# Performance work log

Hardware: AMD Instinct MI355X
Metric: run time of the kernel (lower is better)

Reference implementation:

```python
import jax, jax.numpy as jnp
import numpy as np

KQ_D = 64  # head dim from init_kwargs

def setup_inputs() -> dict:
    key = jax.random.key(0)
    k1, k2, k3, k4 = jax.random.split(key, 4)
    B, H, S, D = 2, 12, 2048, KQ_D
    q = jax.random.normal(k1, (B, H, S, D), dtype=jnp.float32)
    k = jax.random.normal(k2, (B, H, S, D), dtype=jnp.float32)
    v = jax.random.normal(k3, (B, H, S, D), dtype=jnp.float32)
    mask = jax.random.randint(k4, (B, 1, S, S), 0, 2, dtype=jnp.int32)
    return {"q": q, "k": k, "v": v, "mask": mask}

def reference(q, k, v, mask):
    # attn = (q @ k^T) / sqrt(kq_d)
    scale = 1.0 / (KQ_D ** 0.5)
    attn = jnp.einsum('bhqd,bhkd->bhqk', q, k) * scale
    # masked_fill(mask == 0, -1e9)
    attn = jnp.where(mask == 0, jnp.float32(-1e9), attn)
    # softmax over keys; dropout is identity in eval/reference mode
    attn = jax.nn.softmax(attn, axis=-1)
    out = jnp.einsum('bhqk,bhkd->bhqd', attn, v)
    return out
```

## Files before the change

### kernel.cpp

```cpp
#include <hip/hip_runtime.h>
#include <hip/hip_bf16.h>

#define S_LEN 2048
#define D_DIM 64
#define NH    12
#define NB    2
#define BH_N  (NB*NH)
#define TILES 32
#define TILE_BYTES 16384
#define KV_WS_BYTES ((size_t)BH_N * TILES * TILE_BYTES)
#define MASK_WORDS  ((size_t)NB * S_LEN * TILES)
#define WS_NEEDED   (KV_WS_BYTES + MASK_WORDS * 8)

typedef __attribute__((ext_vector_type(8))) short short8;
typedef __attribute__((ext_vector_type(4))) float f32x4;

static __device__ inline unsigned bfbits(float f) {
    __hip_bfloat16 h = __float2bfloat16(f);
    return (unsigned)*reinterpret_cast<const unsigned short*>(&h);
}

static __device__ inline void gload_lds16(const void* g, unsigned ldsoff) {
    __builtin_amdgcn_global_load_lds(
        (__attribute__((address_space(1))) void*)(unsigned long long)(uintptr_t)g,
        (__attribute__((address_space(3))) void*)(unsigned long long)ldsoff,
        16, 0, 0);
}

__global__ __launch_bounds__(256) void prep(const float* __restrict__ k,
                                            const float* __restrict__ v,
                                            const int* __restrict__ mask,
                                            char* __restrict__ wsKV,
                                            unsigned long long* __restrict__ wm) {
    __shared__ __align__(16) float sv[64 * 68];
    const int tid = threadIdx.x;
    const int bid = blockIdx.x;
    if (bid < 768) {
        const int t = bid & 31, bh = bid >> 5;
        const int kv0 = t * 64;
        const float* kb = k + (size_t)bh * (S_LEN * D_DIM);
        const float* vb = v + (size_t)bh * (S_LEN * D_DIM);
        char* img = wsKV + ((size_t)bh * TILES + t) * TILE_BYTES;

#pragma unroll
        for (int g = 0; g < 4; ++g) {
            int i = g * 256 + tid;
            int row = i >> 4, cb = (i & 15) << 3;
            int cp = cb ^ ((row & 7) << 4);
            float4 f = *(const float4*)(kb + (size_t)(kv0 + row) * D_DIM + (cp >> 1));
            uint2 u;
            u.x = bfbits(f.x) | (bfbits(f.y) << 16);
            u.y = bfbits(f.z) | (bfbits(f.w) << 16);
            *(uint2*)(img + (size_t)i * 8) = u;
            float4 fv = *(const float4*)(vb + (size_t)(kv0 + row) * D_DIM + ((i & 15) << 2));
            *(float4*)&sv[row * 68 + ((i & 15) << 2)] = fv;
        }
        __syncthreads();
#pragma unroll
        for (int g = 0; g < 4; ++g) {
            int i = g * 256 + tid;
            int drow = i >> 4, cb = (i & 15) << 3;
            int cp = cb ^ ((drow & 7) << 4);
            int key0 = cp >> 1;
            uint2 u;
            u.x = bfbits(sv[(key0 + 0) * 68 + drow]) | (bfbits(sv[(key0 + 1) * 68 + drow]) << 16);
            u.y = bfbits(sv[(key0 + 2) * 68 + drow]) | (bfbits(sv[(key0 + 3) * 68 + drow]) << 16);
            *(uint2*)(img + 8192 + (size_t)i * 8) = u;
        }
    } else {
        const int lane = tid & 63;
        const int wgid = (bid - 768) * 4 + (tid >> 6);
#pragma unroll 1
        for (int g = 0; g < 16; ++g) {
            const int t0 = wgid * 64 + g * 4;
            const size_t base = (size_t)t0 * 64 + lane;
            int m0 = mask[base];
            int m1 = mask[base + 64];
            int m2 = mask[base + 128];
            int m3 = mask[base + 192];
            unsigned long long b0 = __ballot(m0 != 0);
            unsigned long long b1 = __ballot(m1 != 0);
            unsigned long long b2 = __ballot(m2 != 0);
            unsigned long long b3 = __ballot(m3 != 0);
            if (lane == 0) {
                wm[t0 + 0] = b0; wm[t0 + 1] = b1;
                wm[t0 + 2] = b2; wm[t0 + 3] = b3;
            }
        }
    }
}

__global__ __launch_bounds__(256, 3) void attn_main(
    const float* __restrict__ q, const char* __restrict__ wsKV,
    const unsigned long long* __restrict__ wm, float* __restrict__ out)
{
    __shared__ __align__(16) char smem[2 * TILE_BYTES + 8192];

    const int tid  = threadIdx.x;
    const int wave = tid >> 6;
    const int lane = tid & 63;
    const int l16  = lane & 15;
    const int lhi  = lane >> 4;

    const int f  = blockIdx.x;
    const int n  = (f & 7) * 96 + (f >> 3);
    const int bx = n & 31;
    const int bh = n >> 5;
    const int b  = bh / NH;
    const int qw = bx * 64 + wave * 16;
    const int qq = qw + l16;

    const float* qb = q + (size_t)bh * (S_LEN * D_DIM);
    float*       ob = out + (size_t)bh * (S_LEN * D_DIM);
    const char*  tileBase = wsKV + (size_t)bh * TILES * TILE_BYTES;
    const size_t widx = ((size_t)b * S_LEN + qq) * TILES;

    const float PRE = 0.125f * 1.44269504088896f;

    short8 bq[2];
#pragma unroll
    for (int ks = 0; ks < 2; ++ks) {
        const float* src = qb + (size_t)qq * D_DIM + ks * 32 + lhi * 8;
        float4 f0 = *(const float4*)(src);
        float4 f1 = *(const float4*)(src + 4);
        short8 a;
        a[0] = (short)bfbits(f0.x * PRE); a[1] = (short)bfbits(f0.y * PRE);
        a[2] = (short)bfbits(f0.z * PRE); a[3] = (short)bfbits(f0.w * PRE);
        a[4] = (short)bfbits(f1.x * PRE); a[5] = (short)bfbits(f1.y * PRE);
        a[6] = (short)bfbits(f1.z * PRE); a[7] = (short)bfbits(f1.w * PRE);
        bq[ks] = a;
    }

    f32x4 o[4];
#pragma unroll
    for (int dt = 0; dt < 4; ++dt) o[dt] = (f32x4){0.f, 0.f, 0.f, 0.f};
    float lsum = 0.f;

    const unsigned smem_base = (unsigned)(uintptr_t)(&smem[0]);
    char* pw = smem + 2 * TILE_BYTES + wave * 2048;

    unsigned long long mw = wm[widx];
#pragma unroll
    for (int j = 0; j < 4; ++j) {
        unsigned off = (unsigned)(wave * 4096 + j * 1024 + lane * 16);
        gload_lds16(tileBase + off, smem_base + off);
    }
    __syncthreads();

    int buf = 0;
    for (int t = 0; t < 32; ++t) {
        if (t < 31) {
            const char* timg = tileBase + (size_t)(t + 1) * TILE_BYTES;
            unsigned dstb = smem_base + (unsigned)((buf ^ 1) * TILE_BYTES);
#pragma unroll
            for (int j = 0; j < 4; ++j) {
                unsigned off = (unsigned)(wave * 4096 + j * 1024 + lane * 16);
                gload_lds16(timg + off, dstb + off);
            }
        }
        unsigned long long mw_next = (t < 31) ? wm[widx + t + 1] : 0ull;

        const char* sK  = smem + buf * TILE_BYTES;
        const char* sVt = sK + 8192;

        f32x4 sc[4];
#pragma unroll
        for (int tt = 0; tt < 4; ++tt) sc[tt] = (f32x4){0.f, 0.f, 0.f, 0.f};
#pragma unroll
        for (int ks = 0; ks < 2; ++ks) {
#pragma unroll
            for (int tt = 0; tt < 4; ++tt) {
                int row = tt * 16 + l16;
                int byte = row * 128 + ((ks * 64 + lhi * 16) ^ ((row & 7) << 4));
                short8 ak = *(const short8*)(sK + byte);
                sc[tt] = __builtin_amdgcn_mfma_f32_16x16x32_bf16(ak, bq[ks], sc[tt], 0, 0, 0);
            }
        }

        short8 bvv[2][4];
#pragma unroll
        for (int ks = 0; ks < 2; ++ks)
#pragma unroll
            for (int dt = 0; dt < 4; ++dt) {
                int drow = dt * 16 + l16;
                int vbyte = drow * 128 + ((ks * 64 + lhi * 16) ^ ((drow & 7) << 4));
                bvv[ks][dt] = *(const short8*)(sVt + vbyte);
            }

        float rs = 0.f;
#pragma unroll
        for (int tt = 0; tt < 4; ++tt) {
            unsigned nib = (unsigned)(mw >> (tt * 16 + lhi * 4)) & 0xFu;
#pragma unroll
            for (int r = 0; r < 4; ++r) {
                float s = ((nib >> r) & 1u) ? sc[tt][r] : -1e9f;
                float p = exp2f(s);
                sc[tt][r] = p;
                rs += p;
            }
        }
        lsum += rs;

#pragma unroll
        for (int tt = 0; tt < 4; ++tt) {
            uint2 u;
            u.x = bfbits(sc[tt][0]) | (bfbits(sc[tt][1]) << 16);
            u.y = bfbits(sc[tt][2]) | (bfbits(sc[tt][3]) << 16);
            int byte = l16 * 128 + (((tt * 16 + lhi * 4) * 2) ^ ((l16 & 7) << 4));
            *(uint2*)(pw + byte) = u;
        }

#pragma unroll
        for (int ks = 0; ks < 2; ++ks) {
            int pbyte = l16 * 128 + ((ks * 64 + lhi * 16) ^ ((l16 & 7) << 4));
            short8 pa = *(const short8*)(pw + pbyte);
#pragma unroll
            for (int dt = 0; dt < 4; ++dt)
                o[dt] = __builtin_amdgcn_mfma_f32_16x16x32_bf16(pa, bvv[ks][dt], o[dt], 0, 0, 0);
        }

        __syncthreads();
        buf ^= 1;
        mw = mw_next;
    }

    lsum += __shfl_xor(lsum, 16);
    lsum += __shfl_xor(lsum, 32);
    float invl = 1.0f / lsum;
    float ir[4];
#pragma unroll
    for (int r = 0; r < 4; ++r) ir[r] = __shfl(invl, lhi * 4 + r);
#pragma unroll
    for (int dt = 0; dt < 4; ++dt)
#pragma unroll
        for (int r = 0; r < 4; ++r) {
            int qrow = qw + lhi * 4 + r;
            int dcol = dt * 16 + l16;
            ob[(size_t)qrow * D_DIM + dcol] = o[dt][r] * ir[r];
        }
}

__global__ __launch_bounds__(256, 3) void attn_fallback(
    const float* __restrict__ q, const float* __restrict__ k,
    const float* __restrict__ v, const int* __restrict__ mask,
    float* __restrict__ out)
{
    __shared__ __align__(16) unsigned short sK[4096];
    __shared__ __align__(16) unsigned short sVt[4096];
    __shared__ __align__(16) unsigned short sP[4096];

    const int tid  = threadIdx.x;
    const int wave = tid >> 6;
    const int lane = tid & 63;
    const int l16  = lane & 15;
    const int lhi  = lane >> 4;

    const int bh = blockIdx.y;
    const int b  = bh / NH;
    const int q0 = blockIdx.x * 64;
    const int qw = q0 + wave * 16;
    const int qq = qw + l16;

    const float* qbase = q + (size_t)bh * S_LEN * D_DIM;
    const float* kbase = k + (size_t)bh * S_LEN * D_DIM;
    const float* vbase = v + (size_t)bh * S_LEN * D_DIM;
    const int*   mp = mask + (size_t)b * S_LEN * S_LEN + (size_t)qq * S_LEN;

    const float PRE = 0.125f * 1.44269504088896f;

    short8 bq[2];
#pragma unroll
    for (int ks = 0; ks < 2; ++ks) {
        const float* src = qbase + (size_t)qq * D_DIM + ks * 32 + lhi * 8;
        float4 f0 = *(const float4*)(src);
        float4 f1 = *(const float4*)(src + 4);
        short8 a;
        a[0] = (short)bfbits(f0.x * PRE); a[1] = (short)bfbits(f0.y * PRE);
        a[2] = (short)bfbits(f0.z * PRE); a[3] = (short)bfbits(f0.w * PRE);
        a[4] = (short)bfbits(f1.x * PRE); a[5] = (short)bfbits(f1.y * PRE);
        a[6] = (short)bfbits(f1.z * PRE); a[7] = (short)bfbits(f1.w * PRE);
        bq[ks] = a;
    }

    f32x4 o[4];
#pragma unroll
    for (int dt = 0; dt < 4; ++dt) o[dt] = (f32x4){0.f, 0.f, 0.f, 0.f};
    float mrun = -1e30f, lrun = 0.f;
    unsigned short* pw = sP + wave * 1024;

    int srow[4], sd[4];
#pragma unroll
    for (int s = 0; s < 4; ++s) { int i = tid + 256 * s; srow[s] = i >> 4; sd[s] = (i & 15) * 4; }

    float4 kreg[4], vreg[4];
#pragma unroll
    for (int s = 0; s < 4; ++s) {
        kreg[s] = *(const float4*)(kbase + (size_t)srow[s] * D_DIM + sd[s]);
        vreg[s] = *(const float4*)(vbase + (size_t)srow[s] * D_DIM + sd[s]);
    }

    for (int kv0 = 0; kv0 < S_LEN; kv0 += 64) {
        __syncthreads();
#pragma unroll
        for (int s = 0; s < 4; ++s) {
            unsigned p0 = bfbits(kreg[s].x) | (bfbits(kreg[s].y) << 16);
            unsigned p1 = bfbits(kreg[s].z) | (bfbits(kreg[s].w) << 16);
            int byte = srow[s] * 128 + ((sd[s] * 2) ^ ((srow[s] & 7) << 4));
            *(uint2*)((char*)sK + byte) = make_uint2(p0, p1);
        }
#pragma unroll
        for (int s = 0; s < 4; ++s) {
            float ff[4] = {vreg[s].x, vreg[s].y, vreg[s].z, vreg[s].w};
#pragma unroll
            for (int jj = 0; jj < 4; ++jj) {
                int dd = sd[s] + jj;
                int byte = dd * 128 + ((srow[s] * 2) ^ ((dd & 7) << 4));
                *(unsigned short*)((char*)sVt + byte) = (unsigned short)bfbits(ff[jj]);
            }
        }
        __syncthreads();

        if (kv0 + 64 < S_LEN) {
#pragma unroll
            for (int s = 0; s < 4; ++s) {
                kreg[s] = *(const float4*)(kbase + (size_t)(kv0 + 64 + srow[s]) * D_DIM + sd[s]);
                vreg[s] = *(const float4*)(vbase + (size_t)(kv0 + 64 + srow[s]) * D_DIM + sd[s]);
            }
        }

        int4 m0 = *(const int4*)(mp + kv0 + lhi * 4);
        int4 m1 = *(const int4*)(mp + kv0 + 16 + lhi * 4);
        int4 m2 = *(const int4*)(mp + kv0 + 32 + lhi * 4);
        int4 m3 = *(const int4*)(mp + kv0 + 48 + lhi * 4);

        f32x4 sc[4];
#pragma unroll
        for (int tt = 0; tt < 4; ++tt) sc[tt] = (f32x4){0.f, 0.f, 0.f, 0.f};
#pragma unroll
        for (int ks = 0; ks < 2; ++ks) {
#pragma unroll
            for (int tt = 0; tt < 4; ++tt) {
                int row = tt * 16 + l16;
                int byte = row * 128 + ((ks * 64 + lhi * 16) ^ ((row & 7) << 4));
                short8 ak = *(const short8*)((const char*)sK + byte);
                sc[tt] = __builtin_amdgcn_mfma_f32_16x16x32_bf16(ak, bq[ks], sc[tt], 0, 0, 0);
            }
        }

        const int4 mm[4] = {m0, m1, m2, m3};
        float pm = -1e30f;
#pragma unroll
        for (int tt = 0; tt < 4; ++tt)
#pragma unroll
            for (int r = 0; r < 4; ++r) {
                float s = ((const int*)&mm[tt])[r] ? sc[tt][r] : -1e9f;
                sc[tt][r] = s;
                pm = fmaxf(pm, s);
            }
        pm = fmaxf(pm, __shfl_xor(pm, 16));
        pm = fmaxf(pm, __shfl_xor(pm, 32));

        float mnew = fmaxf(mrun, pm);
        float fsc = exp2f(mrun - mnew);
        mrun = mnew;
        float rs = 0.f;
#pragma unroll
        for (int tt = 0; tt < 4; ++tt)
#pragma unroll
            for (int r = 0; r < 4; ++r) {
                float p = exp2f(sc[tt][r] - mnew);
                sc[tt][r] = p;
                rs += p;
            }
        rs += __shfl_xor(rs, 16);
        rs += __shfl_xor(rs, 32);
        lrun = lrun * fsc + rs;

        float fr[4];
#pragma unroll
        for (int r = 0; r < 4; ++r) fr[r] = __shfl(fsc, lhi * 4 + r);
#pragma unroll
        for (int dt = 0; dt < 4; ++dt)
#pragma unroll
            for (int r = 0; r < 4; ++r) o[dt][r] *= fr[r];

#pragma unroll
        for (int tt = 0; tt < 4; ++tt) {
            unsigned p0 = bfbits(sc[tt][0]) | (bfbits(sc[tt][1]) << 16);
            unsigned p1 = bfbits(sc[tt][2]) | (bfbits(sc[tt][3]) << 16);
            int byte = l16 * 128 + (((tt * 16 + lhi * 4) * 2) ^ ((l16 & 7) << 4));
            *(uint2*)((char*)pw + byte) = make_uint2(p0, p1);
        }

#pragma unroll
        for (int ks = 0; ks < 2; ++ks) {
            int pbyte = l16 * 128 + ((ks * 64 + lhi * 16) ^ ((l16 & 7) << 4));
            short8 pa = *(const short8*)((const char*)pw + pbyte);
#pragma unroll
            for (int dt = 0; dt < 4; ++dt) {
                int drow = dt * 16 + l16;
                int vbyte = drow * 128 + ((ks * 64 + lhi * 16) ^ ((drow & 7) << 4));
                short8 bv = *(const short8*)((const char*)sVt + vbyte);
                o[dt] = __builtin_amdgcn_mfma_f32_16x16x32_bf16(pa, bv, o[dt], 0, 0, 0);
            }
        }
    }

    float invl = 1.0f / lrun;
    float ir[4];
#pragma unroll
    for (int r = 0; r < 4; ++r) ir[r] = __shfl(invl, lhi * 4 + r);
#pragma unroll
    for (int dt = 0; dt < 4; ++dt)
#pragma unroll
        for (int r = 0; r < 4; ++r) {
            int qrow = qw + lhi * 4 + r;
            int dcol = dt * 16 + l16;
            out[(size_t)bh * S_LEN * D_DIM + (size_t)qrow * D_DIM + dcol] = o[dt][r] * ir[r];
        }
}

extern "C" void kernel_launch(void* const* d_in, const int* in_sizes, int n_in,
                              void* d_out, int out_size, void* d_ws, size_t ws_size,
                              hipStream_t stream) {
    const float* q   = (const float*)d_in[0];
    const float* k   = (const float*)d_in[1];
    const float* v   = (const float*)d_in[2];
    const int* mask  = (const int*)d_in[3];
    float* out = (float*)d_out;

    if (ws_size >= WS_NEEDED) {
        char* ws = (char*)d_ws;
        char* wsKV = ws;
        unsigned long long* wm = (unsigned long long*)(ws + KV_WS_BYTES);
        prep<<<dim3(1280), dim3(256), 0, stream>>>(k, v, mask, wsKV, wm);
        attn_main<<<dim3(768), dim3(256), 0, stream>>>(q, wsKV, wm, out);
    } else {
        attn_fallback<<<dim3(S_LEN / 64, BH_N), dim3(256), 0, stream>>>(q, k, v, mask, out);
    }
}
```

Before: 73.55 us.

## Switch attention main loop to 32x32x16 MFMA with split-K waves

Reworks the main attention kernel to use 32x32x16 bf16 MFMA instructions instead of 16x16x32. Waves are now split two ways over query rows and two ways over keys within each tile, and the two key-half partial outputs and row sums are merged through shared memory at the end. Exponentials for masked entries are skipped and P is written directly per group. The aim is fewer, larger MFMAs and fewer LDS reads per tile, at the cost of an extra LDS reduction and a sync in the epilogue.

```diff
diff --git a/kernel.cpp b/kernel.cpp
--- a/kernel.cpp
+++ b/kernel.cpp
@@ -14,6 +14,7 @@
 
 typedef __attribute__((ext_vector_type(8))) short short8;
 typedef __attribute__((ext_vector_type(4))) float f32x4;
+typedef __attribute__((ext_vector_type(16))) float f32x16;
 
 static __device__ inline unsigned bfbits(float f) {
     __hip_bfloat16 h = __float2bfloat16(f);
@@ -99,16 +100,18 @@
     const int tid  = threadIdx.x;
     const int wave = tid >> 6;
     const int lane = tid & 63;
-    const int l16  = lane & 15;
-    const int lhi  = lane >> 4;
+    const int l32  = lane & 31;
+    const int lh   = lane >> 5;
+    const int qh   = wave & 1;
+    const int kh   = wave >> 1;
 
     const int f  = blockIdx.x;
     const int n  = (f & 7) * 96 + (f >> 3);
     const int bx = n & 31;
     const int bh = n >> 5;
     const int b  = bh / NH;
-    const int qw = bx * 64 + wave * 16;
-    const int qq = qw + l16;
+    const int qw = bx * 64 + qh * 32;
+    const int qq = qw + l32;
 
     const float* qb = q + (size_t)bh * (S_LEN * D_DIM);
     float*       ob = out + (size_t)bh * (S_LEN * D_DIM);
@@ -117,10 +120,10 @@
 
     const float PRE = 0.125f * 1.44269504088896f;
 
-    short8 bq[2];
-#pragma unroll
-    for (int ks = 0; ks < 2; ++ks) {
-        const float* src = qb + (size_t)qq * D_DIM + ks * 32 + lhi * 8;
+    short8 bq[4];
+#pragma unroll
+    for (int c = 0; c < 4; ++c) {
+        const float* src = qb + (size_t)qq * D_DIM + c * 16 + lh * 8;
         float4 f0 = *(const float4*)(src);
         float4 f1 = *(const float4*)(src + 4);
         short8 a;
@@ -128,18 +131,22 @@
         a[2] = (short)bfbits(f0.z * PRE); a[3] = (short)bfbits(f0.w * PRE);
         a[4] = (short)bfbits(f1.x * PRE); a[5] = (short)bfbits(f1.y * PRE);
         a[6] = (short)bfbits(f1.z * PRE); a[7] = (short)bfbits(f1.w * PRE);
-        bq[ks] = a;
-    }
-
-    f32x4 o[4];
-#pragma unroll
-    for (int dt = 0; dt < 4; ++dt) o[dt] = (f32x4){0.f, 0.f, 0.f, 0.f};
+        bq[c] = a;
+    }
+
+    f32x16 o0, o1;
+#pragma unroll
+    for (int i = 0; i < 16; ++i) { o0[i] = 0.f; o1[i] = 0.f; }
     float lsum = 0.f;
 
     const unsigned smem_base = (unsigned)(uintptr_t)(&smem[0]);
     char* pw = smem + 2 * TILE_BYTES + wave * 2048;
+    const unsigned swzP = (unsigned)((l32 & 3) << 4);
+    const int krow = kh * 32 + l32;
+    const unsigned kswz = (unsigned)((l32 & 7) << 4);
 
     unsigned long long mw = wm[widx];
+    unsigned long long mwn;
 #pragma unroll
     for (int j = 0; j < 4; ++j) {
         unsigned off = (unsigned)(wave * 4096 + j * 1024 + lane * 16);
@@ -157,87 +164,102 @@
                 unsigned off = (unsigned)(wave * 4096 + j * 1024 + lane * 16);
                 gload_lds16(timg + off, dstb + off);
             }
-        }
-        unsigned long long mw_next = (t < 31) ? wm[widx + t + 1] : 0ull;
+            mwn = wm[widx + t + 1];
+        }
 
         const char* sK  = smem + buf * TILE_BYTES;
         const char* sVt = sK + 8192;
 
-        f32x4 sc[4];
-#pragma unroll
-        for (int tt = 0; tt < 4; ++tt) sc[tt] = (f32x4){0.f, 0.f, 0.f, 0.f};
-#pragma unroll
-        for (int ks = 0; ks < 2; ++ks) {
-#pragma unroll
-            for (int tt = 0; tt < 4; ++tt) {
-                int row = tt * 16 + l16;
-                int byte = row * 128 + ((ks * 64 + lhi * 16) ^ ((row & 7) << 4));
-                short8 ak = *(const short8*)(sK + byte);
-                sc[tt] = __builtin_amdgcn_mfma_f32_16x16x32_bf16(ak, bq[ks], sc[tt], 0, 0, 0);
-            }
-        }
-
-        short8 bvv[2][4];
-#pragma unroll
-        for (int ks = 0; ks < 2; ++ks)
-#pragma unroll
-            for (int dt = 0; dt < 4; ++dt) {
-                int drow = dt * 16 + l16;
-                int vbyte = drow * 128 + ((ks * 64 + lhi * 16) ^ ((drow & 7) << 4));
-                bvv[ks][dt] = *(const short8*)(sVt + vbyte);
-            }
-
+        f32x16 sc;
+#pragma unroll
+        for (int i = 0; i < 16; ++i) sc[i] = 0.f;
+#pragma unroll
+        for (int c = 0; c < 4; ++c) {
+            unsigned byte = (unsigned)(krow * 128) + (((unsigned)(c * 32 + lh * 16)) ^ kswz);
+            short8 ak = *(const short8*)(sK + byte);
+            sc = __builtin_amdgcn_mfma_f32_32x32x16_bf16(ak, bq[c], sc, 0, 0, 0);
+        }
+
+        short8 bv00, bv01, bv10, bv11;
+        {
+            unsigned d0 = (unsigned)(l32 * 128);
+            unsigned d1 = (unsigned)((32 + l32) * 128);
+            unsigned c0 = ((unsigned)(kh * 64 + 0 * 32 + lh * 16)) ^ kswz;
+            unsigned c1 = ((unsigned)(kh * 64 + 1 * 32 + lh * 16)) ^ kswz;
+            bv00 = *(const short8*)(sVt + d0 + c0);
+            bv01 = *(const short8*)(sVt + d1 + c0);
+            bv10 = *(const short8*)(sVt + d0 + c1);
+            bv11 = *(const short8*)(sVt + d1 + c1);
+        }
+
+        unsigned mh = (unsigned)(mw >> (kh * 32 + lh * 4));
         float rs = 0.f;
 #pragma unroll
-        for (int tt = 0; tt < 4; ++tt) {
-            unsigned nib = (unsigned)(mw >> (tt * 16 + lhi * 4)) & 0xFu;
-#pragma unroll
-            for (int r = 0; r < 4; ++r) {
-                float s = ((nib >> r) & 1u) ? sc[tt][r] : -1e9f;
-                float p = exp2f(s);
-                sc[tt][r] = p;
-                rs += p;
-            }
+        for (int g = 0; g < 4; ++g) {
+            unsigned nib = (mh >> (8 * g)) & 0xFu;
+            float p0 = (nib & 1u) ? exp2f(sc[4 * g + 0]) : 0.f;
+            float p1 = (nib & 2u) ? exp2f(sc[4 * g + 1]) : 0.f;
+            float p2 = (nib & 4u) ? exp2f(sc[4 * g + 2]) : 0.f;
+            float p3 = (nib & 8u) ? exp2f(sc[4 * g + 3]) : 0.f;
+            rs += (p0 + p1) + (p2 + p3);
+            uint2 u;
+            u.x = bfbits(p0) | (bfbits(p1) << 16);
+            u.y = bfbits(p2) | (bfbits(p3) << 16);
+            unsigned byte = (unsigned)(l32 * 64) + (((unsigned)(16 * g + 8 * lh)) ^ swzP);
+            *(uint2*)(pw + byte) = u;
         }
         lsum += rs;
 
 #pragma unroll
-        for (int tt = 0; tt < 4; ++tt) {
-            uint2 u;
-            u.x = bfbits(sc[tt][0]) | (bfbits(sc[tt][1]) << 16);
-            u.y = bfbits(sc[tt][2]) | (bfbits(sc[tt][3]) << 16);
-            int byte = l16 * 128 + (((tt * 16 + lhi * 4) * 2) ^ ((l16 & 7) << 4));
-            *(uint2*)(pw + byte) = u;
-        }
-
-#pragma unroll
-        for (int ks = 0; ks < 2; ++ks) {
-            int pbyte = l16 * 128 + ((ks * 64 + lhi * 16) ^ ((l16 & 7) << 4));
+        for (int kc = 0; kc < 2; ++kc) {
+            unsigned pbyte = (unsigned)(l32 * 64) + (((unsigned)(kc * 32 + lh * 16)) ^ swzP);
             short8 pa = *(const short8*)(pw + pbyte);
-#pragma unroll
-            for (int dt = 0; dt < 4; ++dt)
-                o[dt] = __builtin_amdgcn_mfma_f32_16x16x32_bf16(pa, bvv[ks][dt], o[dt], 0, 0, 0);
+            if (kc == 0) {
+                o0 = __builtin_amdgcn_mfma_f32_32x32x16_bf16(pa, bv00, o0, 0, 0, 0);
+                o1 = __builtin_amdgcn_mfma_f32_32x32x16_bf16(pa, bv01, o1, 0, 0, 0);
+            } else {
+                o0 = __builtin_amdgcn_mfma_f32_32x32x16_bf16(pa, bv10, o0, 0, 0, 0);
+                o1 = __builtin_amdgcn_mfma_f32_32x32x16_bf16(pa, bv11, o1, 0, 0, 0);
+            }
         }
 
         __syncthreads();
         buf ^= 1;
-        mw = mw_next;
-    }
-
-    lsum += __shfl_xor(lsum, 16);
+        mw = mwn;
+    }
+
+    float* mO = (float*)smem;
+    float* sl = (float*)(smem + 16384);
+
     lsum += __shfl_xor(lsum, 32);
-    float invl = 1.0f / lsum;
-    float ir[4];
-#pragma unroll
-    for (int r = 0; r < 4; ++r) ir[r] = __shfl(invl, lhi * 4 + r);
-#pragma unroll
-    for (int dt = 0; dt < 4; ++dt)
-#pragma unroll
-        for (int r = 0; r < 4; ++r) {
-            int qrow = qw + lhi * 4 + r;
-            int dcol = dt * 16 + l16;
-            ob[(size_t)qrow * D_DIM + dcol] = o[dt][r] * ir[r];
-        }
+    if (lh == 0) sl[kh * 64 + qh * 32 + l32] = lsum;
+    if (kh == 1) {
+#pragma unroll
+        for (int g = 0; g < 4; ++g)
+#pragma unroll
+            for (int r = 0; r < 4; ++r) {
+                int reg = 4 * g + r;
+                int qrow = r + 8 * g + 4 * lh;
+                mO[qh * 2048 + qrow * 64 + l32]      = o0[reg];
+                mO[qh * 2048 + qrow * 64 + 32 + l32] = o1[reg];
+            }
+    }
+    __syncthreads();
+    if (kh == 0) {
+#pragma unroll
+        for (int g = 0; g < 4; ++g)
+#pragma unroll
+            for (int r = 0; r < 4; ++r) {
+                int reg = 4 * g + r;
+                int qrow = r + 8 * g + 4 * lh;
+                float l = sl[qh * 32 + qrow] + sl[64 + qh * 32 + qrow];
+                float inv = 1.0f / l;
+                float v0 = (o0[reg] + mO[qh * 2048 + qrow * 64 + l32]) * inv;
+                float v1 = (o1[reg] + mO[qh * 2048 + qrow * 64 + 32 + l32]) * inv;
+                ob[(size_t)(qw + qrow) * D_DIM + l32]      = v0;
+                ob[(size_t)(qw + qrow) * D_DIM + 32 + l32] = v1;
+            }
+    }
 }
 
 __global__ __launch_bounds__(256, 3) void attn_fallback(
```

Measured after the change: 81.60 us. +10.9%, slower.

## Software-pipeline QK^T of next tile with softmax/PV of previous tile

Applied to the files above, without the earlier changes.

Restructures the KV tile loop so that the QK^T MFMAs and V fragment loads for tile i run in the same step as the exp, P write-back and PV MFMAs for tile i-1, using ping-pong register sets unrolled by two. This is meant to let independent MFMA and VALU/exp work overlap and hide LDS latency inside each iteration. Masked entries now skip the exp and produce zero directly. The cost is roughly double the live registers for scores and V fragments, which can lower occupancy or cause spills.

```diff
diff --git a/kernel.cpp b/kernel.cpp
--- a/kernel.cpp
+++ b/kernel.cpp
@@ -139,90 +139,111 @@
     const unsigned smem_base = (unsigned)(uintptr_t)(&smem[0]);
     char* pw = smem + 2 * TILE_BYTES + wave * 2048;
 
-    unsigned long long mw = wm[widx];
+    f32x4 scA[4], scB[4];
+    short8 vA[2][4], vB[2][4];
+    unsigned long long mwA, mwB;
+
+#define QKL(SC, VV, RB) { \
+    const char* sK_  = smem + (RB) * TILE_BYTES; \
+    const char* sVt_ = sK_ + 8192; \
+    _Pragma("unroll") \
+    for (int tt = 0; tt < 4; ++tt) SC[tt] = (f32x4){0.f, 0.f, 0.f, 0.f}; \
+    _Pragma("unroll") \
+    for (int ks = 0; ks < 2; ++ks) { \
+        _Pragma("unroll") \
+        for (int tt = 0; tt < 4; ++tt) { \
+            int row = tt * 16 + l16; \
+            int byte = row * 128 + ((ks * 64 + lhi * 16) ^ ((row & 7) << 4)); \
+            short8 ak = *(const short8*)(sK_ + byte); \
+            SC[tt] = __builtin_amdgcn_mfma_f32_16x16x32_bf16(ak, bq[ks], SC[tt], 0, 0, 0); \
+        } \
+    } \
+    _Pragma("unroll") \
+    for (int ks = 0; ks < 2; ++ks) \
+        _Pragma("unroll") \
+        for (int dt = 0; dt < 4; ++dt) { \
+            int drow = dt * 16 + l16; \
+            int vbyte = drow * 128 + ((ks * 64 + lhi * 16) ^ ((drow & 7) << 4)); \
+            VV[ks][dt] = *(const short8*)(sVt_ + vbyte); \
+        } }
+
+#define FIN(SC, VV, MW) { \
+    float rs = 0.f; \
+    _Pragma("unroll") \
+    for (int tt = 0; tt < 4; ++tt) { \
+        unsigned nib = (unsigned)((MW) >> (tt * 16 + lhi * 4)) & 0xFu; \
+        _Pragma("unroll") \
+        for (int r = 0; r < 4; ++r) { \
+            float p = ((nib >> r) & 1u) ? exp2f(SC[tt][r]) : 0.f; \
+            SC[tt][r] = p; \
+            rs += p; \
+        } \
+    } \
+    lsum += rs; \
+    _Pragma("unroll") \
+    for (int tt = 0; tt < 4; ++tt) { \
+        uint2 u; \
+        u.x = bfbits(SC[tt][0]) | (bfbits(SC[tt][1]) << 16); \
+        u.y = bfbits(SC[tt][2]) | (bfbits(SC[tt][3]) << 16); \
+        int byte = l16 * 128 + (((tt * 16 + lhi * 4) * 2) ^ ((l16 & 7) << 4)); \
+        *(uint2*)(pw + byte) = u; \
+    } \
+    _Pragma("unroll") \
+    for (int ks = 0; ks < 2; ++ks) { \
+        int pbyte = l16 * 128 + ((ks * 64 + lhi * 16) ^ ((l16 & 7) << 4)); \
+        short8 pa = *(const short8*)(pw + pbyte); \
+        _Pragma("unroll") \
+        for (int dt = 0; dt < 4; ++dt) \
+            o[dt] = __builtin_amdgcn_mfma_f32_16x16x32_bf16(pa, VV[ks][dt], o[dt], 0, 0, 0); \
+    } }
+
+#define ITER(I_, RB, SCN, VVN, MWN, SCP, VVP, MWP) { \
+    if ((I_) < 31) { \
+        const char* timg = tileBase + (size_t)((I_) + 1) * TILE_BYTES; \
+        unsigned dstb = smem_base + (unsigned)((((I_) + 1) & 1) * TILE_BYTES); \
+        _Pragma("unroll") \
+        for (int j = 0; j < 4; ++j) { \
+            unsigned off = (unsigned)(wave * 4096 + j * 1024 + lane * 16); \
+            gload_lds16(timg + off, dstb + off); \
+        } \
+    } \
+    MWN = wm[widx + (I_)]; \
+    QKL(SCN, VVN, RB) \
+    FIN(SCP, VVP, MWP) \
+    __syncthreads(); }
+
 #pragma unroll
     for (int j = 0; j < 4; ++j) {
         unsigned off = (unsigned)(wave * 4096 + j * 1024 + lane * 16);
         gload_lds16(tileBase + off, smem_base + off);
     }
     __syncthreads();
-
-    int buf = 0;
-    for (int t = 0; t < 32; ++t) {
-        if (t < 31) {
-            const char* timg = tileBase + (size_t)(t + 1) * TILE_BYTES;
-            unsigned dstb = smem_base + (unsigned)((buf ^ 1) * TILE_BYTES);
-#pragma unroll
-            for (int j = 0; j < 4; ++j) {
-                unsigned off = (unsigned)(wave * 4096 + j * 1024 + lane * 16);
-                gload_lds16(timg + off, dstb + off);
-            }
-        }
-        unsigned long long mw_next = (t < 31) ? wm[widx + t + 1] : 0ull;
-
-        const char* sK  = smem + buf * TILE_BYTES;
-        const char* sVt = sK + 8192;
-
-        f32x4 sc[4];
-#pragma unroll
-        for (int tt = 0; tt < 4; ++tt) sc[tt] = (f32x4){0.f, 0.f, 0.f, 0.f};
-#pragma unroll
-        for (int ks = 0; ks < 2; ++ks) {
-#pragma unroll
-            for (int tt = 0; tt < 4; ++tt) {
-                int row = tt * 16 + l16;
-                int byte = row * 128 + ((ks * 64 + lhi * 16) ^ ((row & 7) << 4));
-                short8 ak = *(const short8*)(sK + byte);
-                sc[tt] = __builtin_amdgcn_mfma_f32_16x16x32_bf16(ak, bq[ks], sc[tt], 0, 0, 0);
-            }
-        }
-
-        short8 bvv[2][4];
-#pragma unroll
-        for (int ks = 0; ks < 2; ++ks)
-#pragma unroll
-            for (int dt = 0; dt < 4; ++dt) {
-                int drow = dt * 16 + l16;
-                int vbyte = drow * 128 + ((ks * 64 + lhi * 16) ^ ((drow & 7) << 4));
-                bvv[ks][dt] = *(const short8*)(sVt + vbyte);
-            }
-
-        float rs = 0.f;
-#pragma unroll
-        for (int tt = 0; tt < 4; ++tt) {
-            unsigned nib = (unsigned)(mw >> (tt * 16 + lhi * 4)) & 0xFu;
-#pragma unroll
-            for (int r = 0; r < 4; ++r) {
-                float s = ((nib >> r) & 1u) ? sc[tt][r] : -1e9f;
-                float p = exp2f(s);
-                sc[tt][r] = p;
-                rs += p;
-            }
-        }
-        lsum += rs;
-
-#pragma unroll
-        for (int tt = 0; tt < 4; ++tt) {
-            uint2 u;
-            u.x = bfbits(sc[tt][0]) | (bfbits(sc[tt][1]) << 16);
-            u.y = bfbits(sc[tt][2]) | (bfbits(sc[tt][3]) << 16);
-            int byte = l16 * 128 + (((tt * 16 + lhi * 4) * 2) ^ ((l16 & 7) << 4));
-            *(uint2*)(pw + byte) = u;
-        }
-
-#pragma unroll
-        for (int ks = 0; ks < 2; ++ks) {
-            int pbyte = l16 * 128 + ((ks * 64 + lhi * 16) ^ ((l16 & 7) << 4));
-            short8 pa = *(const short8*)(pw + pbyte);
-#pragma unroll
-            for (int dt = 0; dt < 4; ++dt)
-                o[dt] = __builtin_amdgcn_mfma_f32_16x16x32_bf16(pa, bvv[ks][dt], o[dt], 0, 0, 0);
-        }
-
-        __syncthreads();
-        buf ^= 1;
-        mw = mw_next;
-    }
+    {
+        const char* timg = tileBase + (size_t)1 * TILE_BYTES;
+        unsigned dstb = smem_base + (unsigned)TILE_BYTES;
+#pragma unroll
+        for (int j = 0; j < 4; ++j) {
+            unsigned off = (unsigned)(wave * 4096 + j * 1024 + lane * 16);
+            gload_lds16(timg + off, dstb + off);
+        }
+    }
+    mwA = wm[widx];
+    QKL(scA, vA, 0)
+    __syncthreads();
+
+    int i = 1;
+#pragma unroll 1
+    for (int th = 0; th < 15; ++th) {
+        ITER(i,     1, scB, vB, mwB, scA, vA, mwA)
+        ITER(i + 1, 0, scA, vA, mwA, scB, vB, mwB)
+        i += 2;
+    }
+    ITER(31, 1, scB, vB, mwB, scA, vA, mwA)
+    FIN(scB, vB, mwB)
+
+#undef ITER
+#undef FIN
+#undef QKL
 
     lsum += __shfl_xor(lsum, 16);
     lsum += __shfl_xor(lsum, 32);
```

Measured after the change: 74.19 us. No clear change (+0.9%).
